# Kernel optimization log

Hardware: AMD Instinct MI355X
Metric: run time of the kernel (lower is better)

The kernel has to match this reference:

```python
import jax, jax.numpy as jnp
import numpy as np

E, T, D, H = 4, 4096, 2048, 8192

def setup_inputs() -> dict:
    key = jax.random.key(0)
    k1, k2, k3 = jax.random.split(key, 3)
    x = jax.random.normal(k1, (E, T, D), dtype=jnp.float32)
    fc1_w = jax.random.normal(k2, (E, D, H), dtype=jnp.float32) * 0.001
    fc2_w = jax.random.normal(k3, (E, H, D), dtype=jnp.float32) * 0.001
    fc1_b = jnp.zeros((E, 1, H), dtype=jnp.float32)
    fc2_b = jnp.zeros((E, 1, D), dtype=jnp.float32)
    return {"x": x, "fc1_w": fc1_w, "fc1_b": fc1_b, "fc2_w": fc2_w, "fc2_b": fc2_b}

def reference(x, fc1_w, fc1_b, fc2_w, fc2_b):
    # batched expert FFN: y = relu(x @ W1 + b1) @ W2 + b2, per expert e
    y = jnp.einsum('etd,edh->eth', x, fc1_w) + fc1_b
    y = jax.nn.relu(y)
    y = jnp.einsum('eth,ehd->etd', y, fc2_w) + fc2_b
    return y
```

## Files before the change

### kernel.cpp

```cpp
#include <hip/hip_runtime.h>
#include <hip/hip_bf16.h>
#include <stdint.h>

#define E_ 4
#define T_ 4096
#define D_ 2048
#define H_ 8192

typedef __attribute__((ext_vector_type(8))) short bf16x8;
typedef __attribute__((ext_vector_type(4))) float f32x4;
typedef __attribute__((ext_vector_type(4))) unsigned short u16x4;

__device__ __forceinline__ unsigned short f2bf(float f) {
    unsigned int u = __float_as_uint(f);
    u = u + 0x7fffu + ((u >> 16) & 1u);
    return (unsigned short)(u >> 16);
}

__device__ __forceinline__ void async16(const unsigned short* g, unsigned short* l) {
    auto gp = (const __attribute__((address_space(1))) unsigned int*)g;
    auto lp = (__attribute__((address_space(3))) unsigned int*)l;
    __builtin_amdgcn_global_load_lds(gp, lp, 16, 0, 0);
}

__device__ __forceinline__ f32x4 mfma16(bf16x8 a, bf16x8 b, f32x4 c) {
    return __builtin_amdgcn_mfma_f32_16x16x32_bf16(a, b, c, 0, 0, 0);
}

__global__ void cvt_x_kernel(const float4* __restrict__ in, uint2* __restrict__ out, long n4) {
    long i = (long)blockIdx.x * blockDim.x + threadIdx.x;
    long stride = (long)gridDim.x * blockDim.x;
    for (; i < n4; i += stride) {
        float4 v = in[i];
        uint2 o;
        o.x = (unsigned)f2bf(v.x) | ((unsigned)f2bf(v.y) << 16);
        o.y = (unsigned)f2bf(v.z) | ((unsigned)f2bf(v.w) << 16);
        out[i] = o;
    }
}

__global__ void transpose_cvt_kernel(const float* __restrict__ W, unsigned short* __restrict__ Wt,
                                     int R, int C) {
    __shared__ float tile[64][65];
    const float* Wp = W + (size_t)blockIdx.z * R * C;
    unsigned short* Wtp = Wt + (size_t)blockIdx.z * R * C;
    const int c0 = blockIdx.x * 64, r0 = blockIdx.y * 64;
    const int tc = threadIdx.x & 63;
    const int tr = threadIdx.x >> 6;
#pragma unroll
    for (int i = 0; i < 16; ++i) {
        int r = tr * 16 + i;
        tile[r][tc] = Wp[(size_t)(r0 + r) * C + c0 + tc];
    }
    __syncthreads();
#pragma unroll
    for (int i = 0; i < 16; ++i) {
        int r = tr * 16 + i;
        Wtp[(size_t)(c0 + r) * R + r0 + tc] = f2bf(tile[tc][r]);
    }
}

template <int K, int OUT_MODE>
__global__ __launch_bounds__(512, 2) void gemm256_kernel(
    const unsigned short* __restrict__ A,
    const unsigned short* __restrict__ Bt,
    const float* __restrict__ bias,
    void* __restrict__ Cout,
    int M, int N)
{
    constexpr int BK = 64;
    constexpr int NT = K / BK;
    __shared__ __align__(16) unsigned short L[2][2][2][128][64];

    const int nx = gridDim.x, ny = gridDim.y;
    const int nwg = nx * ny * gridDim.z;
    const int w = (blockIdx.z * ny + blockIdx.y) * nx + blockIdx.x;
    const int cpx = nwg >> 3;
    const int xcd = w & 7;
    const int c = w >> 3;
    const int CR = cpx / nx;
    const int GX = (nx % 16 == 0) ? 16 : nx;
    const int g = c / (GX * CR);
    const int r1 = c - g * (GX * CR);
    const int byl = r1 / GX;
    const int bxi = r1 - byl * GX;
    const int fy = xcd * CR + byl;
    const int bx = g * GX + bxi;
    const int e = fy / ny;
    const int by = fy - e * ny;

    const unsigned short* Ae = A + (size_t)e * M * K;
    const unsigned short* Be = Bt + (size_t)e * N * K;
    const int bm0 = by * 256;
    const int bn0 = bx * 256;

    const int tid = threadIdx.x;
    const int lane = tid & 63;
    const int wid = tid >> 6;
    const int wr = wid >> 2;
    const int wc = wid & 3;

    const int srow8 = wid * 8 + (lane >> 3);
    const int skel = 8 * ((lane & 7) ^ (lane >> 3));
    const unsigned short* Abase = Ae + (size_t)(bm0 + srow8) * K + skel;
    const unsigned short* Bbase = Be + (size_t)(bn0 + srow8) * K + skel;

#define STG_A(S_, T_, H_, RO_) \
    async16(Abase + ((size_t)((H_) * 128 + (RO_)) * K + (T_) * BK), \
            &L[S_][0][H_][(RO_) + wid * 8][0])
#define STG_B(S_, T_, H_, RO_) \
    async16(Bbase + ((size_t)((H_) * 128 + (RO_)) * K + (T_) * BK), \
            &L[S_][1][H_][(RO_) + wid * 8][0])

    const int fr = lane & 15;
    const int kq = lane >> 4;
    const int ksw = (lane & 7) << 3;
    const int bh = wc >> 1;
    const int brb = (wc & 1) * 64;

#define RD_A(S_, MOFF_) \
    _Pragma("unroll") for (int m = 0; m < 4; ++m) \
    _Pragma("unroll") for (int kk = 0; kk < 2; ++kk) \
        a[m][kk] = *(const bf16x8*)&L[S_][0][wr][(m + (MOFF_)) * 16 + fr][(kk * 32 + kq * 8) ^ ksw]
#define RD_B(S_, N0_, N1_) \
    _Pragma("unroll") for (int n = (N0_); n < (N1_); ++n) \
    _Pragma("unroll") for (int kk = 0; kk < 2; ++kk) \
        b[n][kk] = *(const bf16x8*)&L[S_][1][bh][brb + n * 16 + fr][(kk * 32 + kq * 8) ^ ksw]

#define CLOSEBAR do { __builtin_amdgcn_s_barrier(); __builtin_amdgcn_sched_barrier(0); } while (0)
#define MFMA_Q(MB_, NB_) do { __builtin_amdgcn_s_setprio(1); \
    _Pragma("unroll") for (int m = 0; m < 4; ++m) \
    _Pragma("unroll") for (int n = 0; n < 2; ++n) \
    _Pragma("unroll") for (int kk = 0; kk < 2; ++kk) \
        acc[(MB_) + m][(NB_) + n] = mfma16(a[m][kk], b[(NB_) + n][kk], acc[(MB_) + m][(NB_) + n]); \
    __builtin_amdgcn_s_setprio(0); } while (0)

    f32x4 acc[8][4] = {};
    bf16x8 a[4][2], b[4][2];

    STG_A(0, 0, 0, 0);  STG_A(0, 0, 1, 0);
    STG_B(0, 0, 0, 0);  STG_B(0, 0, 0, 64);
    STG_B(0, 0, 1, 0);  STG_B(0, 0, 1, 64);
    STG_A(0, 0, 0, 64); STG_A(0, 0, 1, 64);
    STG_A(1, 1, 0, 0);  STG_A(1, 1, 1, 0);
    STG_B(1, 1, 0, 0);  STG_B(1, 1, 0, 64);
    STG_B(1, 1, 1, 0);  STG_B(1, 1, 1, 64);
    asm volatile("s_waitcnt vmcnt(6)" ::: "memory");
    __builtin_amdgcn_sched_barrier(0);
    __builtin_amdgcn_s_barrier();
    RD_B(0, 0, 2);

#define ITER(NOTLAST_) do { \
        const int tA = 2 * j, tB = tA + 1; \
         \
        RD_A(0, 0); \
        STG_A(1, tB, 0, 64); STG_A(1, tB, 1, 64); \
        __builtin_amdgcn_sched_barrier(0); \
        MFMA_Q(0, 0); \
        RD_B(0, 2, 4); \
        CLOSEBAR; \
         \
        if (NOTLAST_) { STG_A(0, tA + 2, 0, 0); STG_A(0, tA + 2, 1, 0); } \
        __builtin_amdgcn_sched_barrier(0); \
        MFMA_Q(0, 2); \
        RD_A(0, 4); \
        CLOSEBAR; \
         \
        if (NOTLAST_) { STG_B(0, tA + 2, 0, 0); STG_B(0, tA + 2, 0, 64); } \
        __builtin_amdgcn_sched_barrier(0); \
        MFMA_Q(4, 0); \
        CLOSEBAR; \
         \
        if (NOTLAST_) { STG_B(0, tA + 2, 1, 0); STG_B(0, tA + 2, 1, 64); } \
        if (NOTLAST_) { asm volatile("s_waitcnt vmcnt(6)" ::: "memory"); } \
        else         { asm volatile("s_waitcnt vmcnt(0)" ::: "memory"); } \
        __builtin_amdgcn_sched_barrier(0); \
        RD_B(1, 0, 2); \
        MFMA_Q(4, 2); \
        CLOSEBAR; \
         \
        RD_A(1, 0); \
        if (NOTLAST_) { STG_A(0, tA + 2, 0, 64); STG_A(0, tA + 2, 1, 64); } \
        __builtin_amdgcn_sched_barrier(0); \
        MFMA_Q(0, 0); \
        RD_B(1, 2, 4); \
        CLOSEBAR; \
         \
        if (NOTLAST_) { STG_A(1, tB + 2, 0, 0); STG_A(1, tB + 2, 1, 0); } \
        __builtin_amdgcn_sched_barrier(0); \
        MFMA_Q(0, 2); \
        RD_A(1, 4); \
        CLOSEBAR; \
         \
        if (NOTLAST_) { STG_B(1, tB + 2, 0, 0); STG_B(1, tB + 2, 0, 64); } \
        __builtin_amdgcn_sched_barrier(0); \
        MFMA_Q(4, 0); \
        CLOSEBAR; \
         \
        if (NOTLAST_) { STG_B(1, tB + 2, 1, 0); STG_B(1, tB + 2, 1, 64); } \
        if (NOTLAST_) { asm volatile("s_waitcnt vmcnt(6)" ::: "memory"); } \
        else         { asm volatile("s_waitcnt vmcnt(0)" ::: "memory"); } \
        __builtin_amdgcn_sched_barrier(0); \
        if (NOTLAST_) { RD_B(0, 0, 2); } \
        MFMA_Q(4, 2); \
        CLOSEBAR; \
    } while (0)

    for (int j = 0; j < NT / 2 - 1; ++j) { ITER(true); }
    { const int j = NT / 2 - 1; ITER(false); }

#undef ITER
#undef MFMA_Q
#undef CLOSEBAR
#undef RD_A
#undef RD_B
#undef STG_A
#undef STG_B

    constexpr int ST = 260;
    float* S = (float*)&L[0][0][0][0][0];
    const int rowq = (lane >> 4) * 4;
    const float* bp = bias + (size_t)e * N;
    const float4 bb4 = *(const float4*)(bp + bn0 + lane * 4);

    unsigned short* Y = (unsigned short*)Cout + (size_t)e * M * N;
    float* O = (float*)Cout + (size_t)e * M * N;

#pragma unroll
    for (int sg = 0; sg < 8; ++sg) {
        __syncthreads();
        if (wr == (sg >> 2)) {
            const int sl = sg & 3;
#pragma unroll
            for (int mm = 0; mm < 2; ++mm) {
#pragma unroll
                for (int n = 0; n < 4; ++n) {
#pragma unroll
                    for (int j2 = 0; j2 < 4; ++j2) {
                        S[(mm * 16 + rowq + j2) * ST + wc * 64 + n * 16 + fr] =
                            acc[2 * sl + mm][n][j2];
                    }
                }
            }
        }
        __syncthreads();
#pragma unroll
        for (int rr = 0; rr < 4; ++rr) {
            const int rl = wid * 4 + rr;
            const int rg = bm0 + sg * 32 + rl;
            f32x4 v = *(const f32x4*)&S[rl * ST + lane * 4];
            v[0] += bb4.x; v[1] += bb4.y; v[2] += bb4.z; v[3] += bb4.w;
            if (OUT_MODE == 0) {
                u16x4 o;
                o[0] = f2bf(fmaxf(v[0], 0.0f));
                o[1] = f2bf(fmaxf(v[1], 0.0f));
                o[2] = f2bf(fmaxf(v[2], 0.0f));
                o[3] = f2bf(fmaxf(v[3], 0.0f));
                *(u16x4*)(Y + (size_t)rg * N + bn0 + lane * 4) = o;
            } else {
                *(f32x4*)(O + (size_t)rg * N + bn0 + lane * 4) = v;
            }
        }
    }
}

extern "C" void kernel_launch(void* const* d_in, const int* in_sizes, int n_in,
                              void* d_out, int out_size, void* d_ws, size_t ws_size,
                              hipStream_t stream) {
    const float* x     = (const float*)d_in[0];
    const float* fc1_w = (const float*)d_in[1];
    const float* fc1_b = (const float*)d_in[2];
    const float* fc2_w = (const float*)d_in[3];
    const float* fc2_b = (const float*)d_in[4];
    float* out = (float*)d_out;

    const size_t n_x  = (size_t)E_ * T_ * D_;
    const size_t n_w1 = (size_t)E_ * D_ * H_;
    const size_t n_w2 = (size_t)E_ * H_ * D_;
    const size_t n_y1 = (size_t)E_ * T_ * H_;

    const size_t need = (n_x + n_w1 + n_w2 + n_y1) * sizeof(unsigned short);
    if (ws_size < need) return;

    unsigned short* xb  = (unsigned short*)d_ws;
    unsigned short* w1t = xb + n_x;
    unsigned short* w2t = w1t + n_w1;
    unsigned short* y1  = w2t + n_w2;

    cvt_x_kernel<<<2048, 256, 0, stream>>>((const float4*)x, (uint2*)xb, (long)(n_x / 4));
    {
        dim3 g(H_ / 64, D_ / 64, E_);
        transpose_cvt_kernel<<<g, 256, 0, stream>>>(fc1_w, w1t, D_, H_);
    }
    {
        dim3 g(D_ / 64, H_ / 64, E_);
        transpose_cvt_kernel<<<g, 256, 0, stream>>>(fc2_w, w2t, H_, D_);
    }
    {
        dim3 g(H_ / 256, T_ / 256, E_);
        gemm256_kernel<D_, 0><<<g, 512, 0, stream>>>(xb, w1t, fc1_b, (void*)y1, T_, H_);
    }
    {
        dim3 g(D_ / 256, T_ / 256, E_);
        gemm256_kernel<H_, 1><<<g, 512, 0, stream>>>(y1, w2t, fc2_b, (void*)out, T_, D_);
    }
}
```

Measured before the change: 1.076 ms.

## Double-buffer A fragments in registers to overlap LDS reads with MFMAs

Adds a second register fragment set for A so that the next A half-tile is read from LDS while MFMAs run on the current one, rather than reading A just before it is used. The next stage's B and A reads are moved one phase earlier, and the vmcnt wait is placed earlier and tightened from 6 to 4 outstanding loads to match. This is meant to hide LDS read latency behind matrix math, but it raises VGPR pressure, which may lower occupancy or cause spills, and it changes when global loads must have completed.

```diff
diff --git a/kernel.cpp b/kernel.cpp
--- a/kernel.cpp
+++ b/kernel.cpp
@@ -118,25 +118,25 @@
     const int bh = wc >> 1;
     const int brb = (wc & 1) * 64;
 
-#define RD_A(S_, MOFF_) \
-    _Pragma("unroll") for (int m = 0; m < 4; ++m) \
+#define RD_AF(S_, ARR_, MOFF_, M0_, M1_) \
+    _Pragma("unroll") for (int m = (M0_); m < (M1_); ++m) \
     _Pragma("unroll") for (int kk = 0; kk < 2; ++kk) \
-        a[m][kk] = *(const bf16x8*)&L[S_][0][wr][(m + (MOFF_)) * 16 + fr][(kk * 32 + kq * 8) ^ ksw]
+        ARR_[m][kk] = *(const bf16x8*)&L[S_][0][wr][(m + (MOFF_)) * 16 + fr][(kk * 32 + kq * 8) ^ ksw]
 #define RD_B(S_, N0_, N1_) \
     _Pragma("unroll") for (int n = (N0_); n < (N1_); ++n) \
     _Pragma("unroll") for (int kk = 0; kk < 2; ++kk) \
         b[n][kk] = *(const bf16x8*)&L[S_][1][bh][brb + n * 16 + fr][(kk * 32 + kq * 8) ^ ksw]
 
 #define CLOSEBAR do { __builtin_amdgcn_s_barrier(); __builtin_amdgcn_sched_barrier(0); } while (0)
-#define MFMA_Q(MB_, NB_) do { __builtin_amdgcn_s_setprio(1); \
+#define MFMA_Q(ARR_, MB_, NB_) do { __builtin_amdgcn_s_setprio(1); \
     _Pragma("unroll") for (int m = 0; m < 4; ++m) \
     _Pragma("unroll") for (int n = 0; n < 2; ++n) \
     _Pragma("unroll") for (int kk = 0; kk < 2; ++kk) \
-        acc[(MB_) + m][(NB_) + n] = mfma16(a[m][kk], b[(NB_) + n][kk], acc[(MB_) + m][(NB_) + n]); \
+        acc[(MB_) + m][(NB_) + n] = mfma16(ARR_[m][kk], b[(NB_) + n][kk], acc[(MB_) + m][(NB_) + n]); \
     __builtin_amdgcn_s_setprio(0); } while (0)
 
     f32x4 acc[8][4] = {};
-    bf16x8 a[4][2], b[4][2];
+    bf16x8 a[4][2], ah[4][2], b[4][2];
 
     STG_A(0, 0, 0, 0);  STG_A(0, 0, 1, 0);
     STG_B(0, 0, 0, 0);  STG_B(0, 0, 0, 64);
@@ -149,60 +149,64 @@
     __builtin_amdgcn_sched_barrier(0);
     __builtin_amdgcn_s_barrier();
     RD_B(0, 0, 2);
+    RD_AF(0, a, 0, 0, 4);
 
 #define ITER(NOTLAST_) do { \
         const int tA = 2 * j, tB = tA + 1; \
          \
-        RD_A(0, 0); \
         STG_A(1, tB, 0, 64); STG_A(1, tB, 1, 64); \
         __builtin_amdgcn_sched_barrier(0); \
-        MFMA_Q(0, 0); \
+        MFMA_Q(a, 0, 0); \
         RD_B(0, 2, 4); \
+        RD_AF(0, ah, 4, 0, 1); \
         CLOSEBAR; \
          \
         if (NOTLAST_) { STG_A(0, tA + 2, 0, 0); STG_A(0, tA + 2, 1, 0); } \
         __builtin_amdgcn_sched_barrier(0); \
-        MFMA_Q(0, 2); \
-        RD_A(0, 4); \
+        MFMA_Q(a, 0, 2); \
+        RD_AF(0, ah, 4, 1, 4); \
         CLOSEBAR; \
          \
         if (NOTLAST_) { STG_B(0, tA + 2, 0, 0); STG_B(0, tA + 2, 0, 64); } \
-        __builtin_amdgcn_sched_barrier(0); \
-        MFMA_Q(4, 0); \
+        if (NOTLAST_) { asm volatile("s_waitcnt vmcnt(4)" ::: "memory"); } \
+        else         { asm volatile("s_waitcnt vmcnt(0)" ::: "memory"); } \
+        __builtin_amdgcn_sched_barrier(0); \
+        MFMA_Q(ah, 4, 0); \
+        RD_B(1, 0, 2); \
+        RD_AF(1, a, 0, 0, 1); \
         CLOSEBAR; \
          \
         if (NOTLAST_) { STG_B(0, tA + 2, 1, 0); STG_B(0, tA + 2, 1, 64); } \
-        if (NOTLAST_) { asm volatile("s_waitcnt vmcnt(6)" ::: "memory"); } \
+        __builtin_amdgcn_sched_barrier(0); \
+        MFMA_Q(ah, 4, 2); \
+        RD_AF(1, a, 0, 1, 4); \
+        CLOSEBAR; \
+         \
+        if (NOTLAST_) { STG_A(0, tA + 2, 0, 64); STG_A(0, tA + 2, 1, 64); } \
+        __builtin_amdgcn_sched_barrier(0); \
+        MFMA_Q(a, 0, 0); \
+        RD_B(1, 2, 4); \
+        RD_AF(1, ah, 4, 0, 1); \
+        CLOSEBAR; \
+         \
+        if (NOTLAST_) { STG_A(1, tB + 2, 0, 0); STG_A(1, tB + 2, 1, 0); } \
+        __builtin_amdgcn_sched_barrier(0); \
+        MFMA_Q(a, 0, 2); \
+        RD_AF(1, ah, 4, 1, 4); \
+        CLOSEBAR; \
+         \
+        if (NOTLAST_) { STG_B(1, tB + 2, 0, 0); STG_B(1, tB + 2, 0, 64); } \
+        if (NOTLAST_) { asm volatile("s_waitcnt vmcnt(4)" ::: "memory"); } \
         else         { asm volatile("s_waitcnt vmcnt(0)" ::: "memory"); } \
         __builtin_amdgcn_sched_barrier(0); \
-        RD_B(1, 0, 2); \
-        MFMA_Q(4, 2); \
-        CLOSEBAR; \
-         \
-        RD_A(1, 0); \
-        if (NOTLAST_) { STG_A(0, tA + 2, 0, 64); STG_A(0, tA + 2, 1, 64); } \
-        __builtin_amdgcn_sched_barrier(0); \
-        MFMA_Q(0, 0); \
-        RD_B(1, 2, 4); \
-        CLOSEBAR; \
-         \
-        if (NOTLAST_) { STG_A(1, tB + 2, 0, 0); STG_A(1, tB + 2, 1, 0); } \
-        __builtin_amdgcn_sched_barrier(0); \
-        MFMA_Q(0, 2); \
-        RD_A(1, 4); \
-        CLOSEBAR; \
-         \
-        if (NOTLAST_) { STG_B(1, tB + 2, 0, 0); STG_B(1, tB + 2, 0, 64); } \
-        __builtin_amdgcn_sched_barrier(0); \
-        MFMA_Q(4, 0); \
+        MFMA_Q(ah, 4, 0); \
+        if (NOTLAST_) { RD_B(0, 0, 2); RD_AF(0, a, 0, 0, 1); } \
         CLOSEBAR; \
          \
         if (NOTLAST_) { STG_B(1, tB + 2, 1, 0); STG_B(1, tB + 2, 1, 64); } \
-        if (NOTLAST_) { asm volatile("s_waitcnt vmcnt(6)" ::: "memory"); } \
-        else         { asm volatile("s_waitcnt vmcnt(0)" ::: "memory"); } \
-        __builtin_amdgcn_sched_barrier(0); \
-        if (NOTLAST_) { RD_B(0, 0, 2); } \
-        MFMA_Q(4, 2); \
+        __builtin_amdgcn_sched_barrier(0); \
+        MFMA_Q(ah, 4, 2); \
+        if (NOTLAST_) { RD_AF(0, a, 0, 1, 4); } \
         CLOSEBAR; \
     } while (0)
 
@@ -212,7 +216,7 @@
 #undef ITER
 #undef MFMA_Q
 #undef CLOSEBAR
-#undef RD_A
+#undef RD_AF
 #undef RD_B
 #undef STG_A
 #undef STG_B
```

Measured after the change: 1.087 ms. No clear change (+1.1%).
